# Performance work log

Hardware: AMD Instinct MI355X
Metric: run time of the kernel (lower is better)

## Reference

```python
import jax, jax.numpy as jnp
import numpy as np

B, S, E, H = 2, 2048, 1024, 16
D = E // H
SCALE = D ** -0.5


def setup_inputs() -> dict:
    key = jax.random.key(0)
    k1, k2, k3, k4, k5 = jax.random.split(key, 5)
    x = jax.random.normal(k1, (B, S, E), dtype=jnp.float32)
    # torch Linear weights: [out, in]
    W_attn = jax.random.normal(k2, (3 * E, E), dtype=jnp.float32) * (E ** -0.5)
    b_attn = jax.random.normal(k3, (3 * E,), dtype=jnp.float32) * 0.02
    W_proj = jax.random.normal(k4, (E, E), dtype=jnp.float32) * (E ** -0.5)
    b_proj = jax.random.normal(k5, (E,), dtype=jnp.float32) * 0.02
    mask = jnp.tril(jnp.ones((S, S), dtype=jnp.int32))[None, None]  # causal [1,1,S,S]
    return {"x": x, "W_attn": W_attn, "b_attn": b_attn,
            "W_proj": W_proj, "b_proj": b_proj, "mask": mask}


def reference(x, W_attn, b_attn, W_proj, b_proj, mask):
    # fused qkv projection: [B,S,3E]
    qkv = jnp.einsum('bse,fe->bsf', x, W_attn) + b_attn
    q, k, v = jnp.split(qkv, 3, axis=-1)
    # split heads -> [B,H,S,D]
    def heads(t):
        return t.reshape(B, S, H, D).transpose(0, 2, 1, 3)
    q, k, v = heads(q), heads(k), heads(v)
    # scaled dot-product attention with causal mask
    w = jnp.einsum('bhqd,bhkd->bhqk', q, k) * SCALE
    w = jnp.where(mask == 0, jnp.finfo(w.dtype).min, w)
    w = jax.nn.softmax(w, axis=-1)  # attn dropout p=0 (eval)
    o = jnp.einsum('bhqk,bhkd->bhqd', w, v)
    # merge heads -> [B,S,E]
    o = o.transpose(0, 2, 1, 3).reshape(B, S, E)
    out = jnp.einsum('bse,fe->bsf', o, W_proj) + b_proj  # resid dropout p=0
    return out
```

## Files before the change

kernel.cpp:

```cpp
#include <hip/hip_runtime.h>
#include <hip/hip_bf16.h>

typedef unsigned short u16;
typedef unsigned int u32;
typedef float f32x4 __attribute__((ext_vector_type(4)));
typedef short bf16x8 __attribute__((ext_vector_type(8)));

#define BB 2
#define SS 2048
#define EE 1024
#define HH 16
#define DD 64
#define QSCALE 0.18033688011f

__device__ __forceinline__ u16 f2bf(float f) {
    union { u32 i; float f; } x; x.f = f;
    return (u16)((x.i + 0x7FFFu + ((x.i >> 16) & 1u)) >> 16);
}
__device__ __forceinline__ u32 pkbf(float a, float b) {
    __hip_bfloat162 h = __float22bfloat162_rn(make_float2(a, b));
    union { __hip_bfloat162 h; u32 u; } c; c.h = h; return c.u;
}

#define MFMA16(a, b, c) __builtin_amdgcn_mfma_f32_16x16x32_bf16((a), (b), (c), 0, 0, 0)

__device__ __forceinline__ void gld16(const u16* g, u16* l) {
    __builtin_amdgcn_global_load_lds(
        (const __attribute__((address_space(1))) void*)g,
        (__attribute__((address_space(3))) void*)l,
        16, 0, 0);
}

__global__ __launch_bounds__(256) void convert_all(
    const float* __restrict__ x, const float* __restrict__ wa,
    const float* __restrict__ wp, u16* __restrict__ dst)
{
    const size_t n0 = (size_t)4096 * 1024;
    const size_t n1 = n0 + (size_t)3072 * 1024;
    size_t i = ((size_t)blockIdx.x * 256 + threadIdx.x) * 4;
    const float* s;
    size_t off;
    if (i < n0)      { s = x;  off = 0;  }
    else if (i < n1) { s = wa; off = n0; }
    else             { s = wp; off = n1; }
    float4 v = *(const float4*)(s + (i - off));
    uint2 o;
    o.x = pkbf(v.x, v.y);
    o.y = pkbf(v.z, v.w);
    *(uint2*)(dst + i) = o;
}

#define GEMM_CORE(Aptr, Bptr, m0, n0)                                          \
    __shared__ __align__(16) u16 As[128 * 64];                                 \
    __shared__ __align__(16) u16 Bs[128 * 64];                                 \
    const int tid = threadIdx.x;                                               \
    const int wave = tid >> 6, lane = tid & 63;                                \
    const int l16 = lane & 15, quad = lane >> 4;                               \
    const int wm = wave >> 1, wn = wave & 1;                                   \
    const int ldr = lane >> 3;                                                 \
    const int csw = ((lane & 7) ^ ldr) * 8;      \
    f32x4 acc[4][4];                                                           \
    _Pragma("unroll") for (int i = 0; i < 4; ++i)                              \
        _Pragma("unroll") for (int j = 0; j < 4; ++j)                          \
            acc[i][j] = f32x4{0.f, 0.f, 0.f, 0.f};                             \
    for (int k0 = 0; k0 < 1024; k0 += 64) {                                    \
        __syncthreads();                                                       \
        _Pragma("unroll") for (int t = 0; t < 4; ++t) {                        \
            const int a0 = wave * 4 + t;                                       \
            const int row = a0 * 8 + ldr;                                      \
            gld16(Aptr + (size_t)(m0 + row) * 1024 + k0 + csw,                 \
                  &As[a0 * 512 + lane * 8]);                                   \
            gld16(Bptr + (size_t)(n0 + row) * 1024 + k0 + csw,                 \
                  &Bs[a0 * 512 + lane * 8]);                                   \
        }                                                                      \
        __syncthreads();                                                       \
        _Pragma("unroll") for (int ks = 0; ks < 2; ++ks) {                     \
            bf16x8 af[4], bf[4];                                               \
            _Pragma("unroll") for (int i = 0; i < 4; ++i)                      \
                af[i] = *(const bf16x8*)&As[(wm * 64 + i * 16 + l16) * 64 +    \
                                            ((ks * 4 + quad) ^ (l16 & 7)) * 8]; \
            _Pragma("unroll") for (int j = 0; j < 4; ++j)                      \
                bf[j] = *(const bf16x8*)&Bs[(wn * 64 + j * 16 + l16) * 64 +    \
                                            ((ks * 4 + quad) ^ (l16 & 7)) * 8]; \
            _Pragma("unroll") for (int i = 0; i < 4; ++i)                      \
                _Pragma("unroll") for (int j = 0; j < 4; ++j)                  \
                    acc[i][j] = MFMA16(af[i], bf[j], acc[i][j]);               \
        }                                                                      \
    }

__global__ __launch_bounds__(256) void gemm_qkv(
    const u16* __restrict__ A, const u16* __restrict__ B, const float* __restrict__ bias,
    u16* __restrict__ Qo, u16* __restrict__ Ko, u16* __restrict__ Vto)
{
    __shared__ __align__(16) u16 T[128 * 76];
    const int n0 = blockIdx.x * 128, m0 = blockIdx.y * 128;
    GEMM_CORE(A, B, m0, n0)
    const int part = blockIdx.x >> 3;
    if (part != 2) {
        const int h = ((blockIdx.x & 7) << 1) | wn;
#pragma unroll
        for (int j = 0; j < 4; ++j) {
            const int f = n0 + wn * 64 + j * 16 + l16;
            const int d = j * 16 + l16;
            const float bj = bias[f];
#pragma unroll
            for (int i = 0; i < 4; ++i) {
#pragma unroll
                for (int r = 0; r < 4; ++r) {
                    const int m = m0 + wm * 64 + i * 16 + quad * 4 + r;
                    const int b = m >> 11, s = m & 2047;
                    const float val = acc[i][j][r] + bj;
                    if (part == 0)
                        Qo[(((size_t)(b * HH + h)) * SS + s) * DD + d] = f2bf(val * QSCALE);
                    else
                        Ko[(((size_t)(b * HH + h)) * SS + s) * DD + d] = f2bf(val);
                }
            }
        }
    } else {
        const int hbase = (blockIdx.x & 7) << 1;
#pragma unroll
        for (int wmr = 0; wmr < 2; ++wmr) {
            __syncthreads();
            if (wm == wmr) {
#pragma unroll
                for (int j = 0; j < 4; ++j) {
                    const float bj = bias[n0 + wn * 64 + j * 16 + l16];
#pragma unroll
                    for (int i = 0; i < 4; ++i) {
                        uint2 pw;
                        pw.x = pkbf(acc[i][j][0] + bj, acc[i][j][1] + bj);
                        pw.y = pkbf(acc[i][j][2] + bj, acc[i][j][3] + bj);
                        *(uint2*)&T[(wn * 64 + j * 16 + l16) * 76 + i * 16 + quad * 4] = pw;
                    }
                }
            }
            __syncthreads();
            const int frow = tid >> 1;
            const int h = hbase + (frow >> 6);
            const int d = frow & 63;
            const int mg = m0 + wmr * 64;
            const int b = mg >> 11, sbase = mg & 2047;
            u16* dstrow = Vto + (((size_t)(b * HH + h)) * DD + d) * SS + sbase;
#pragma unroll
            for (int l = 0; l < 8; ++l) {
                const int mo = (tid & 1) * 32 + l * 4;
                *(uint2*)(dstrow + mo) = *(const uint2*)&T[frow * 76 + mo];
            }
        }
    }
}

__global__ __launch_bounds__(256) void gemm_proj(
    const u16* __restrict__ A, const u16* __restrict__ B, const float* __restrict__ bias,
    float* __restrict__ out)
{
    const int n0 = blockIdx.x * 128, m0 = blockIdx.y * 128;
    GEMM_CORE(A, B, m0, n0)
#pragma unroll
    for (int j = 0; j < 4; ++j) {
        const int f = n0 + wn * 64 + j * 16 + l16;
        const float bj = bias[f];
#pragma unroll
        for (int i = 0; i < 4; ++i) {
#pragma unroll
            for (int r = 0; r < 4; ++r) {
                const int m = m0 + wm * 64 + i * 16 + quad * 4 + r;
                out[(size_t)m * EE + f] = acc[i][j][r] + bj;
            }
        }
    }
}

__global__ __launch_bounds__(256, 4) void attn(
    const u16* __restrict__ Q, const u16* __restrict__ K, const u16* __restrict__ VT,
    u16* __restrict__ O)
{
    const int qb = 31 - (int)blockIdx.x;
    const int bh = blockIdx.y;
    const int tid = threadIdx.x;
    const int wave = tid >> 6, lane = tid & 63;
    const int l16 = lane & 15, quad = lane >> 4;
    const int ldr = lane >> 3;
    const int csw = ((lane & 7) ^ ldr) * 8;
    __shared__ __align__(16) u16 Ks[64 * 64];
    __shared__ __align__(16) u16 Vts[64 * 64];
    __shared__ __align__(16) u16 Ps[64 * 72];

    const u16* qptr = Q + (size_t)bh * SS * DD;
    const u16* kptr = K + (size_t)bh * SS * DD;
    const u16* vtptr = VT + (size_t)bh * DD * SS;

    const int qrow = qb * 64 + wave * 16 + l16;
    bf16x8 bq[2];
#pragma unroll
    for (int ks = 0; ks < 2; ++ks)
        bq[ks] = *(const bf16x8*)(qptr + (size_t)qrow * DD + ks * 32 + quad * 8);

    float lp = 0.f;
    f32x4 o_acc[4];
#pragma unroll
    for (int j = 0; j < 4; ++j) o_acc[j] = f32x4{0.f, 0.f, 0.f, 0.f};

    for (int kb = 0; kb <= qb; ++kb) {
        const int k0 = kb * 64;
        __syncthreads();
#pragma unroll
        for (int t = 0; t < 2; ++t) {
            const int a0 = wave * 2 + t;
            const int row = a0 * 8 + ldr;
            gld16(kptr + (size_t)(k0 + row) * DD + csw, &Ks[a0 * 512 + lane * 8]);
            gld16(vtptr + (size_t)row * SS + k0 + csw, &Vts[a0 * 512 + lane * 8]);
        }
        __syncthreads();

        f32x4 s[4];
#pragma unroll
        for (int j = 0; j < 4; ++j) s[j] = f32x4{0.f, 0.f, 0.f, 0.f};
#pragma unroll
        for (int ks = 0; ks < 2; ++ks) {
#pragma unroll
            for (int j = 0; j < 4; ++j) {
                bf16x8 ak = *(const bf16x8*)&Ks[(j * 16 + l16) * 64 +
                                                ((ks * 4 + quad) ^ (l16 & 7)) * 8];
                s[j] = MFMA16(ak, bq[ks], s[j]);
            }
        }

        if (kb == qb) {
#pragma unroll
            for (int j = 0; j < 4; ++j)
#pragma unroll
                for (int r = 0; r < 4; ++r) {
                    const int key = k0 + j * 16 + quad * 4 + r;
                    if (key > qrow) s[j][r] = -INFINITY;
                }
        }
#pragma unroll
        for (int j = 0; j < 4; ++j) {
            const float p0 = __builtin_amdgcn_exp2f(s[j][0]);
            const float p1 = __builtin_amdgcn_exp2f(s[j][1]);
            const float p2 = __builtin_amdgcn_exp2f(s[j][2]);
            const float p3 = __builtin_amdgcn_exp2f(s[j][3]);
            lp += (p0 + p1) + (p2 + p3);
            uint2 pw; pw.x = pkbf(p0, p1); pw.y = pkbf(p2, p3);
            *(uint2*)&Ps[(wave * 16 + l16) * 72 + j * 16 + quad * 4] = pw;
        }

#pragma unroll
        for (int ks = 0; ks < 2; ++ks) {
            bf16x8 bp = *(const bf16x8*)&Ps[(wave * 16 + l16) * 72 + ks * 32 + quad * 8];
#pragma unroll
            for (int j = 0; j < 4; ++j) {
                bf16x8 av = *(const bf16x8*)&Vts[(j * 16 + l16) * 64 +
                                                 ((ks * 4 + quad) ^ (l16 & 7)) * 8];
                o_acc[j] = MFMA16(av, bp, o_acc[j]);
            }
        }
    }

    const int b = bh >> 4, h = bh & 15;
    float l = lp;
    l += __shfl_xor(l, 16);
    l += __shfl_xor(l, 32);
    const float inv = 1.0f / l;
#pragma unroll
    for (int j = 0; j < 4; ++j) {
        uint2 o4;
        o4.x = pkbf(o_acc[j][0] * inv, o_acc[j][1] * inv);
        o4.y = pkbf(o_acc[j][2] * inv, o_acc[j][3] * inv);
        *(uint2*)&O[((size_t)(b * SS + qrow)) * EE + h * DD + j * 16 + quad * 4] = o4;
    }
}

extern "C" void kernel_launch(void* const* d_in, const int* in_sizes, int n_in,
                              void* d_out, int out_size, void* d_ws, size_t ws_size,
                              hipStream_t stream) {
    const float* x      = (const float*)d_in[0];
    const float* W_attn = (const float*)d_in[1];
    const float* b_attn = (const float*)d_in[2];
    const float* W_proj = (const float*)d_in[3];
    const float* b_proj = (const float*)d_in[4];
    float* out = (float*)d_out;

    u16* xb  = (u16*)d_ws;
    u16* wab = xb + (size_t)4096 * 1024;
    u16* wpb = wab + (size_t)3072 * 1024;
    u16* qw  = wpb + (size_t)1024 * 1024;
    u16* kw  = qw + (size_t)BB * HH * SS * DD;
    u16* vtw = kw + (size_t)BB * HH * SS * DD;
    u16* ow  = xb;

    convert_all<<<8192, 256, 0, stream>>>(x, W_attn, W_proj, xb);
    gemm_qkv<<<dim3(24, 32), 256, 0, stream>>>(xb, wab, b_attn, qw, kw, vtw);
    attn<<<dim3(32, 32), 256, 0, stream>>>(qw, kw, vtw, ow);
    gemm_proj<<<dim3(8, 32), 256, 0, stream>>>(ow, wpb, b_proj, out);
}
```

Baseline: 213.8 us.

## Use 512-thread blocks with smaller per-wave tiles in both GEMMs

Both GEMM kernels now launch 8 waves per block instead of 4. Each wave computes a 64x32 (QKV) or 32x32 (proj) sub-tile, so it holds fewer accumulator registers, and the waves split the global-to-LDS staging between A and B. The projection GEMM also drops to 64-row M tiles, doubling its grid so more blocks cover the GPU. The V-transpose staging buffer is aliased onto the GEMM shared memory with a padded stride of 72, reducing the LDS footprint. This trades less per-wave reuse and more LDS reads per MFMA for higher occupancy and better latency hiding.

New measurement: 200.7 us. 6.1% less time.

```diff
diff --git a/kernel.cpp b/kernel.cpp
--- a/kernel.cpp
+++ b/kernel.cpp
@@ -50,58 +50,69 @@
     *(uint2*)(dst + i) = o;
 }
 
-#define GEMM_CORE(Aptr, Bptr, m0, n0)                                          \
-    __shared__ __align__(16) u16 As[128 * 64];                                 \
-    __shared__ __align__(16) u16 Bs[128 * 64];                                 \
-    const int tid = threadIdx.x;                                               \
-    const int wave = tid >> 6, lane = tid & 63;                                \
-    const int l16 = lane & 15, quad = lane >> 4;                               \
-    const int wm = wave >> 1, wn = wave & 1;                                   \
-    const int ldr = lane >> 3;                                                 \
-    const int csw = ((lane & 7) ^ ldr) * 8;      \
-    f32x4 acc[4][4];                                                           \
-    _Pragma("unroll") for (int i = 0; i < 4; ++i)                              \
-        _Pragma("unroll") for (int j = 0; j < 4; ++j)                          \
-            acc[i][j] = f32x4{0.f, 0.f, 0.f, 0.f};                             \
-    for (int k0 = 0; k0 < 1024; k0 += 64) {                                    \
-        __syncthreads();                                                       \
-        _Pragma("unroll") for (int t = 0; t < 4; ++t) {                        \
-            const int a0 = wave * 4 + t;                                       \
-            const int row = a0 * 8 + ldr;                                      \
-            gld16(Aptr + (size_t)(m0 + row) * 1024 + k0 + csw,                 \
-                  &As[a0 * 512 + lane * 8]);                                   \
-            gld16(Bptr + (size_t)(n0 + row) * 1024 + k0 + csw,                 \
-                  &Bs[a0 * 512 + lane * 8]);                                   \
-        }                                                                      \
-        __syncthreads();                                                       \
-        _Pragma("unroll") for (int ks = 0; ks < 2; ++ks) {                     \
-            bf16x8 af[4], bf[4];                                               \
-            _Pragma("unroll") for (int i = 0; i < 4; ++i)                      \
-                af[i] = *(const bf16x8*)&As[(wm * 64 + i * 16 + l16) * 64 +    \
-                                            ((ks * 4 + quad) ^ (l16 & 7)) * 8]; \
-            _Pragma("unroll") for (int j = 0; j < 4; ++j)                      \
-                bf[j] = *(const bf16x8*)&Bs[(wn * 64 + j * 16 + l16) * 64 +    \
-                                            ((ks * 4 + quad) ^ (l16 & 7)) * 8]; \
-            _Pragma("unroll") for (int i = 0; i < 4; ++i)                      \
-                _Pragma("unroll") for (int j = 0; j < 4; ++j)                  \
-                    acc[i][j] = MFMA16(af[i], bf[j], acc[i][j]);               \
-        }                                                                      \
-    }
-
-__global__ __launch_bounds__(256) void gemm_qkv(
+__global__ __launch_bounds__(512, 4) void gemm_qkv(
     const u16* __restrict__ A, const u16* __restrict__ B, const float* __restrict__ bias,
     u16* __restrict__ Qo, u16* __restrict__ Ko, u16* __restrict__ Vto)
 {
-    __shared__ __align__(16) u16 T[128 * 76];
+    __shared__ __align__(16) u16 SMEM[16384];
+    u16* As = SMEM;
+    u16* Bs = SMEM + 8192;
     const int n0 = blockIdx.x * 128, m0 = blockIdx.y * 128;
-    GEMM_CORE(A, B, m0, n0)
+    const int tid = threadIdx.x;
+    const int wave = tid >> 6, lane = tid & 63;
+    const int l16 = lane & 15, quad = lane >> 4;
+    const int wm = wave >> 2, wn = wave & 3;
+    const int ldr = lane >> 3;
+    const int csw = ((lane & 7) ^ ldr) * 8;
+
+    f32x4 acc[4][2];
+#pragma unroll
+    for (int i = 0; i < 4; ++i)
+#pragma unroll
+        for (int j = 0; j < 2; ++j) acc[i][j] = f32x4{0.f, 0.f, 0.f, 0.f};
+
+    const int aorb = wave >> 2;
+    u16* stgbuf = aorb ? Bs : As;
+    const u16* stgsrc = aorb ? B : A;
+    const int stgbase = aorb ? n0 : m0;
+
+    for (int k0 = 0; k0 < 1024; k0 += 64) {
+        __syncthreads();
+#pragma unroll
+        for (int t = 0; t < 4; ++t) {
+            const int c = (wave & 3) * 4 + t;
+            const int row = c * 8 + ldr;
+            gld16(stgsrc + (size_t)(stgbase + row) * 1024 + k0 + csw,
+                  &stgbuf[c * 512 + lane * 8]);
+        }
+        __syncthreads();
+#pragma unroll
+        for (int ks = 0; ks < 2; ++ks) {
+            bf16x8 af[4], bf[2];
+#pragma unroll
+            for (int i = 0; i < 4; ++i)
+                af[i] = *(const bf16x8*)&As[(wm * 64 + i * 16 + l16) * 64 +
+                                            ((ks * 4 + quad) ^ (l16 & 7)) * 8];
+#pragma unroll
+            for (int j = 0; j < 2; ++j)
+                bf[j] = *(const bf16x8*)&Bs[(wn * 32 + j * 16 + l16) * 64 +
+                                            ((ks * 4 + quad) ^ (l16 & 7)) * 8];
+#pragma unroll
+            for (int i = 0; i < 4; ++i)
+#pragma unroll
+                for (int j = 0; j < 2; ++j)
+                    acc[i][j] = MFMA16(af[i], bf[j], acc[i][j]);
+        }
+    }
+
     const int part = blockIdx.x >> 3;
+    const int hbase = (blockIdx.x & 7) << 1;
     if (part != 2) {
-        const int h = ((blockIdx.x & 7) << 1) | wn;
-#pragma unroll
-        for (int j = 0; j < 4; ++j) {
-            const int f = n0 + wn * 64 + j * 16 + l16;
-            const int d = j * 16 + l16;
+        const int h = hbase + (wn >> 1);
+#pragma unroll
+        for (int j = 0; j < 2; ++j) {
+            const int f = n0 + wn * 32 + j * 16 + l16;
+            const int d = f & 63;
             const float bj = bias[f];
 #pragma unroll
             for (int i = 0; i < 4; ++i) {
@@ -118,54 +129,103 @@
             }
         }
     } else {
-        const int hbase = (blockIdx.x & 7) << 1;
+        u16* T = SMEM;
 #pragma unroll
         for (int wmr = 0; wmr < 2; ++wmr) {
             __syncthreads();
             if (wm == wmr) {
 #pragma unroll
-                for (int j = 0; j < 4; ++j) {
-                    const float bj = bias[n0 + wn * 64 + j * 16 + l16];
+                for (int j = 0; j < 2; ++j) {
+                    const float bj = bias[n0 + wn * 32 + j * 16 + l16];
 #pragma unroll
                     for (int i = 0; i < 4; ++i) {
                         uint2 pw;
                         pw.x = pkbf(acc[i][j][0] + bj, acc[i][j][1] + bj);
                         pw.y = pkbf(acc[i][j][2] + bj, acc[i][j][3] + bj);
-                        *(uint2*)&T[(wn * 64 + j * 16 + l16) * 76 + i * 16 + quad * 4] = pw;
+                        *(uint2*)&T[(wn * 32 + j * 16 + l16) * 72 + i * 16 + quad * 4] = pw;
                     }
                 }
             }
             __syncthreads();
-            const int frow = tid >> 1;
+            const int frow = tid >> 2;
+            const int qtr = tid & 3;
             const int h = hbase + (frow >> 6);
             const int d = frow & 63;
             const int mg = m0 + wmr * 64;
             const int b = mg >> 11, sbase = mg & 2047;
             u16* dstrow = Vto + (((size_t)(b * HH + h)) * DD + d) * SS + sbase;
 #pragma unroll
-            for (int l = 0; l < 8; ++l) {
-                const int mo = (tid & 1) * 32 + l * 4;
-                *(uint2*)(dstrow + mo) = *(const uint2*)&T[frow * 76 + mo];
-            }
-        }
-    }
-}
-
-__global__ __launch_bounds__(256) void gemm_proj(
+            for (int l = 0; l < 4; ++l) {
+                const int mo = qtr * 16 + l * 4;
+                *(uint2*)(dstrow + mo) = *(const uint2*)&T[frow * 72 + mo];
+            }
+        }
+    }
+}
+
+__global__ __launch_bounds__(512, 4) void gemm_proj(
     const u16* __restrict__ A, const u16* __restrict__ B, const float* __restrict__ bias,
     float* __restrict__ out)
 {
-    const int n0 = blockIdx.x * 128, m0 = blockIdx.y * 128;
-    GEMM_CORE(A, B, m0, n0)
-#pragma unroll
-    for (int j = 0; j < 4; ++j) {
-        const int f = n0 + wn * 64 + j * 16 + l16;
+    __shared__ __align__(16) u16 SMEM[12288];
+    u16* As = SMEM;
+    u16* Bs = SMEM + 4096;
+    const int n0 = blockIdx.x * 128, m0 = blockIdx.y * 64;
+    const int tid = threadIdx.x;
+    const int wave = tid >> 6, lane = tid & 63;
+    const int l16 = lane & 15, quad = lane >> 4;
+    const int wm = wave >> 2, wn = wave & 3;
+    const int ldr = lane >> 3;
+    const int csw = ((lane & 7) ^ ldr) * 8;
+
+    f32x4 acc[2][2];
+#pragma unroll
+    for (int i = 0; i < 2; ++i)
+#pragma unroll
+        for (int j = 0; j < 2; ++j) acc[i][j] = f32x4{0.f, 0.f, 0.f, 0.f};
+
+    for (int k0 = 0; k0 < 1024; k0 += 64) {
+        __syncthreads();
+#pragma unroll
+        for (int t = 0; t < 3; ++t) {
+            const int c = wave * 3 + t;
+            if (c < 8) {
+                const int row = c * 8 + ldr;
+                gld16(A + (size_t)(m0 + row) * 1024 + k0 + csw, &As[c * 512 + lane * 8]);
+            } else {
+                const int c2 = c - 8;
+                const int row = c2 * 8 + ldr;
+                gld16(B + (size_t)(n0 + row) * 1024 + k0 + csw, &Bs[c2 * 512 + lane * 8]);
+            }
+        }
+        __syncthreads();
+#pragma unroll
+        for (int ks = 0; ks < 2; ++ks) {
+            bf16x8 af[2], bf[2];
+#pragma unroll
+            for (int i = 0; i < 2; ++i)
+                af[i] = *(const bf16x8*)&As[(wm * 32 + i * 16 + l16) * 64 +
+                                            ((ks * 4 + quad) ^ (l16 & 7)) * 8];
+#pragma unroll
+            for (int j = 0; j < 2; ++j)
+                bf[j] = *(const bf16x8*)&Bs[(wn * 32 + j * 16 + l16) * 64 +
+                                            ((ks * 4 + quad) ^ (l16 & 7)) * 8];
+#pragma unroll
+            for (int i = 0; i < 2; ++i)
+#pragma unroll
+                for (int j = 0; j < 2; ++j)
+                    acc[i][j] = MFMA16(af[i], bf[j], acc[i][j]);
+        }
+    }
+#pragma unroll
+    for (int j = 0; j < 2; ++j) {
+        const int f = n0 + wn * 32 + j * 16 + l16;
         const float bj = bias[f];
 #pragma unroll
-        for (int i = 0; i < 4; ++i) {
+        for (int i = 0; i < 2; ++i) {
 #pragma unroll
             for (int r = 0; r < 4; ++r) {
-                const int m = m0 + wm * 64 + i * 16 + quad * 4 + r;
+                const int m = m0 + wm * 32 + i * 16 + quad * 4 + r;
                 out[(size_t)m * EE + f] = acc[i][j][r] + bj;
             }
         }
@@ -292,7 +352,7 @@
     u16* ow  = xb;
 
     convert_all<<<8192, 256, 0, stream>>>(x, W_attn, W_proj, xb);
-    gemm_qkv<<<dim3(24, 32), 256, 0, stream>>>(xb, wab, b_attn, qw, kw, vtw);
+    gemm_qkv<<<dim3(24, 32), 512, 0, stream>>>(xb, wab, b_attn, qw, kw, vtw);
     attn<<<dim3(32, 32), 256, 0, stream>>>(qw, kw, vtw, ow);
-    gemm_proj<<<dim3(8, 32), 256, 0, stream>>>(ow, wpb, b_proj, out);
-}
+    gemm_proj<<<dim3(8, 64), 512, 0, stream>>>(ow, wpb, b_proj, out);
+}
```
